# Performance work log

Measured on AMD Instinct MI355X. Metric: run time of the kernel, lower is better.

## Reference

```python
import jax, jax.numpy as jnp
import numpy as np

B, V, C, A = 32, 48, 24, 6
NC, D, H, OUT = 10000, 128, 128, 167


def setup_inputs() -> dict:
    key = jax.random.key(0)
    ks = jax.random.split(key, 12)
    seqs = jax.random.randint(ks[0], (B, V, C), 0, NC + 1)
    ancestors = jax.random.randint(ks[1], (B, V, C, A), 0, NC + 1)
    length = jax.random.randint(ks[2], (B,), 1, V + 1)
    amask = (jax.random.uniform(ks[3], (B, V, C, A)) < 0.7).astype(jnp.float32)
    amask = amask.at[..., 0].set(1.0)  # first ancestor always valid
    emb = jax.random.normal(ks[4], (NC + 1, D), dtype=jnp.float32) * 0.02
    emb = emb.at[NC].set(0.0)  # padding row is zeros
    w_basic = jax.random.normal(ks[5], (D, 2 * D), dtype=jnp.float32) * (1.0 / np.sqrt(2 * D))
    u_basic_w = jax.random.normal(ks[6], (1, D), dtype=jnp.float32) * (1.0 / np.sqrt(D))
    u_basic_b = jnp.zeros((1,), jnp.float32)
    gru_wih = jax.random.normal(ks[7], (3 * H, D), dtype=jnp.float32) * (1.0 / np.sqrt(H))
    gru_whh = jax.random.normal(ks[8], (3 * H, H), dtype=jnp.float32) * (1.0 / np.sqrt(H))
    gru_bih = jnp.zeros((3 * H,), jnp.float32)
    gru_bhh = jnp.zeros((3 * H,), jnp.float32)
    out_w = jax.random.normal(ks[9], (OUT, H), dtype=jnp.float32) * (1.0 / np.sqrt(H))
    out_b = jnp.zeros((OUT,), jnp.float32)
    return dict(seqs=seqs, ancestors=ancestors, length=length, ancestor_length=amask,
                emb=emb, w_basic=w_basic, u_basic_w=u_basic_w, u_basic_b=u_basic_b,
                gru_wih=gru_wih, gru_whh=gru_whh, gru_bih=gru_bih, gru_bhh=gru_bhh,
                out_w=out_w, out_b=out_b)


def _gram_forward(seqs, ancestors, length, ancestor_length, emb, w_basic,
                  u_basic_w, u_basic_b, gru_wih, gru_whh, gru_bih, gru_bhh,
                  out_w, out_b):
    # gather embeddings
    seqs_e = emb[seqs]            # [B,V,C,D]
    anc_e = emb[ancestors]        # [B,V,C,A,D]
    seqs_rep = jnp.broadcast_to(seqs_e[..., None, :], anc_e.shape)
    # Bahdanau attention: mask applied to concat BEFORE the linear (as in source)
    cat = jnp.concatenate([seqs_rep, anc_e], axis=-1) * ancestor_length[..., None]  # [B,V,C,A,2D]
    hdd = jnp.tanh(jnp.einsum('bvcad,ed->bvcae', cat, w_basic))  # [B,V,C,A,D]
    score = jnp.einsum('bvcad,od->bvcao', hdd, u_basic_w) + u_basic_b  # [B,V,C,A,1]
    # mask_softmax over ancestor axis, faithful to the source (sum==0 -> -1)
    e = jnp.exp(score) * ancestor_length[..., None]
    s = jnp.sum(e, axis=3, keepdims=True)
    s = jnp.where(s == 0, -1.0, s)
    attn = e / s                  # [B,V,C,A,1]
    ctx = jnp.sum(attn * anc_e, axis=3)            # [B,V,C,D] weighted ancestor sum
    x = jnp.tanh(jnp.sum(ctx, axis=2))             # [B,V,D] visit embedding

    # single-layer GRU over visits (valid steps form a prefix, padded tail masked below)
    hsz = gru_whh.shape[1]
    def step(hstate, xt):
        gi = xt @ gru_wih.T + gru_bih              # [B,3H]
        gh = hstate @ gru_whh.T + gru_bhh
        ir, iz, inn = jnp.split(gi, 3, axis=-1)
        hr, hz, hn = jnp.split(gh, 3, axis=-1)
        r = jax.nn.sigmoid(ir + hr)
        z = jax.nn.sigmoid(iz + hz)
        n = jnp.tanh(inn + r * hn)
        hnew = (1.0 - z) * n + z * hstate
        return hnew, hnew
    h0 = jnp.zeros((x.shape[0], hsz), x.dtype)
    _, outs = jax.lax.scan(step, h0, jnp.swapaxes(x, 0, 1))  # [V,B,H]
    outs = jnp.swapaxes(outs, 0, 1)                          # [B,V,H]

    visit_mask = (jnp.arange(x.shape[1])[None, :] < length[:, None]).astype(x.dtype)
    context = jnp.einsum('bv,bvh->bh', visit_mask, outs)     # masked sum over visits
    logit = jax.nn.sigmoid(context @ out_w.T + out_b)        # dropout=eval (identity)
    return logit


def reference(seqs, ancestors, length, ancestor_length, emb, w_basic, u_basic_w,
              u_basic_b, gru_wih, gru_whh, gru_bih, gru_bhh, out_w, out_b):
    return _gram_forward(seqs, ancestors, length, ancestor_length, emb, w_basic,
                         u_basic_w, u_basic_b, gru_wih, gru_whh, gru_bih, gru_bhh,
                         out_w, out_b)
```

## Files before the change

### kernel.cpp

```cpp
#include <hip/hip_runtime.h>

#define BB 32
#define VV 48
#define CC 24
#define AA 6
#define NCODES 10001
#define DD 128
#define HH 128
#define OUTN 167
#define G3 384

typedef float f32x4 __attribute__((ext_vector_type(4)));

__device__ __forceinline__ float fast_tanh(float x) {
    return 1.0f - 2.0f / (1.0f + __expf(2.0f * x));
}
__device__ __forceinline__ float fast_sigmoid(float x) {
    return 1.0f / (1.0f + __expf(-x));
}
__device__ __forceinline__ float dot4(float4 a, float4 b) {
    return a.x * b.x + a.y * b.y + a.z * b.z + a.w * b.w;
}
__device__ __forceinline__ float dot4v(f32x4 a, f32x4 b) {
    return a.x * b.x + a.y * b.y + a.z * b.z + a.w * b.w;
}

__global__ __launch_bounds__(256) void k_precompute(
    const float* __restrict__ emb, const float* __restrict__ w_basic,
    float* __restrict__ P1, float* __restrict__ P2, int nrows)
{
    int row0 = blockIdx.x * 16;
    int t = threadIdx.x;
    int tc = t & 127, grp = t >> 7;
    int rbase = row0 + grp * 8;
    const float4* w4 = (const float4*)w_basic;
    const float4* e4 = (const float4*)emb;
    float a0[8] = {}, a1[8] = {};
#pragma unroll 2
    for (int d4 = 0; d4 < 32; ++d4) {
        float4 wv0 = w4[tc * 64 + d4];
        float4 wv1 = w4[tc * 64 + 32 + d4];
#pragma unroll
        for (int r = 0; r < 8; ++r) {
            int row = rbase + r;
            if (row >= nrows) row = nrows - 1;
            float4 ev = e4[row * 32 + d4];
            a0[r] += dot4(ev, wv0);
            a1[r] += dot4(ev, wv1);
        }
    }
#pragma unroll
    for (int r = 0; r < 8; ++r) {
        int row = rbase + r;
        if (row < nrows) {
            P1[row * 128 + tc] = a0[r];
            P2[row * 128 + tc] = a1[r];
        }
    }
}

__global__ __launch_bounds__(256) void k_attention(
    const int* __restrict__ seqs, const int* __restrict__ ancestors,
    const float* __restrict__ amask, const float* __restrict__ emb,
    const float* __restrict__ P1, const float* __restrict__ P2,
    const float* __restrict__ u_w, const float* __restrict__ u_b,
    float* __restrict__ x_out)
{
    __shared__ __align__(16) float u_s[128];
    __shared__ float sc_s[144];
    __shared__ float m_s[144];
    __shared__ int   anc_s[144];
    __shared__ float attn_s[144];
    __shared__ float sum_s[24];
    __shared__ float xred[256];
    int bv = blockIdx.x;
    int t = threadIdx.x;
    if (t < 128) u_s[t] = u_w[t];
    __syncthreads();
    float ub = u_b[0];
    int g = t >> 2, l = t & 3;
    for (int p = g; p < CC * AA; p += 64) {
        int c = p / AA, a = p - c * AA;
        int sidx = bv * CC + c;
        int s_code = seqs[sidx];
        int aidx = sidx * AA + a;
        int anc = ancestors[aidx];
        float m = amask[aidx];
        const float4* p14 = (const float4*)(P1 + s_code * 128);
        const float4* p24 = (const float4*)(P2 + anc * 128);
        const float4* u4 = (const float4*)u_s;
        float partial = 0.0f;
        int e4 = l * 8;
#pragma unroll 2
        for (int j = 0; j < 8; ++j) {
            float4 av = p14[e4 + j];
            float4 bv_ = p24[e4 + j];
            float4 uv = u4[e4 + j];
            partial += fast_tanh(m * (av.x + bv_.x)) * uv.x;
            partial += fast_tanh(m * (av.y + bv_.y)) * uv.y;
            partial += fast_tanh(m * (av.z + bv_.z)) * uv.z;
            partial += fast_tanh(m * (av.w + bv_.w)) * uv.w;
        }
        partial += __shfl_xor(partial, 1);
        partial += __shfl_xor(partial, 2);
        if (l == 0) {
            sc_s[p] = partial + ub;
            m_s[p] = m;
            anc_s[p] = anc;
        }
    }
    __syncthreads();
    if (t < CC * AA) attn_s[t] = __expf(sc_s[t]) * m_s[t];
    __syncthreads();
    if (t < CC) {
        float s = 0.0f;
#pragma unroll
        for (int a = 0; a < AA; ++a) s += attn_s[t * AA + a];
        sum_s[t] = (s == 0.0f) ? -1.0f : s;
    }
    __syncthreads();
    if (t < CC * AA) attn_s[t] = attn_s[t] / sum_s[t / AA];
    __syncthreads();
    int e = t & 127, hc = t >> 7;
    float acc = 0.0f;
    for (int c = hc * 12; c < hc * 12 + 12; ++c) {
#pragma unroll
        for (int a = 0; a < AA; ++a) {
            int p = c * AA + a;
            acc += attn_s[p] * emb[anc_s[p] * 128 + e];
        }
    }
    xred[t] = acc;
    __syncthreads();
    if (t < 128) {
        x_out[bv * 128 + t] = fast_tanh(xred[t] + xred[t + 128]);
    }
}

__global__ __launch_bounds__(384) void k_gi(
    const float* __restrict__ x, const float* __restrict__ wih,
    const float* __restrict__ bih, float* __restrict__ gi)
{
    int row0 = blockIdx.x * 8;
    int t = threadIdx.x;
    const float4* w4 = (const float4*)(wih + t * 128);
    const float4* x4 = (const float4*)(x + row0 * 128);
    float acc[8] = {};
#pragma unroll 2
    for (int d4 = 0; d4 < 32; ++d4) {
        float4 wv = w4[d4];
#pragma unroll
        for (int r = 0; r < 8; ++r) {
            acc[r] += dot4(x4[r * 32 + d4], wv);
        }
    }
    float bb = bih[t];
#pragma unroll
    for (int r = 0; r < 8; ++r) gi[(row0 + r) * G3 + t] = acc[r] + bb;
}

#define GL4(dst, base, OFF) \
    asm volatile("global_load_dwordx4 %0, %1, off offset:" #OFF \
                 : "=v"(dst) : "v"(base))

__global__ __launch_bounds__(256, 1) void k_gru(
    const float* __restrict__ gi, const float* __restrict__ whh,
    const float* __restrict__ bhh, const int* __restrict__ length,
    const float* __restrict__ out_w, const float* __restrict__ out_b,
    float* __restrict__ out)
{
    __shared__ __align__(16) float gl[24 * G3];
    __shared__ __align__(16) float hs[2][128];
    __shared__ __align__(16) float ctxs[128];
    int b = blockIdx.x;
    int t = threadIdx.x;
    int o = t >> 1, half = t & 1;

    const f32x4* bwr = (const f32x4*)(whh + o * 128 + half * 64);
    const f32x4* bwz = (const f32x4*)(whh + (128 + o) * 128 + half * 64);
    const f32x4* bwn = (const f32x4*)(whh + (256 + o) * 128 + half * 64);

    f32x4 wr0, wr1, wr2, wr3, wr4, wr5, wr6, wr7,
          wr8, wr9, wr10, wr11, wr12, wr13, wr14, wr15;
    f32x4 wz0, wz1, wz2, wz3, wz4, wz5, wz6, wz7,
          wz8, wz9, wz10, wz11, wz12, wz13, wz14, wz15;
    f32x4 wn0, wn1, wn2, wn3, wn4, wn5, wn6, wn7,
          wn8, wn9, wn10, wn11, wn12, wn13, wn14, wn15;

    GL4(wr0,  bwr, 0);   GL4(wr1,  bwr, 16);  GL4(wr2,  bwr, 32);  GL4(wr3,  bwr, 48);
    GL4(wr4,  bwr, 64);  GL4(wr5,  bwr, 80);  GL4(wr6,  bwr, 96);  GL4(wr7,  bwr, 112);
    GL4(wr8,  bwr, 128); GL4(wr9,  bwr, 144); GL4(wr10, bwr, 160); GL4(wr11, bwr, 176);
    GL4(wr12, bwr, 192); GL4(wr13, bwr, 208); GL4(wr14, bwr, 224); GL4(wr15, bwr, 240);
    GL4(wz0,  bwz, 0);   GL4(wz1,  bwz, 16);  GL4(wz2,  bwz, 32);  GL4(wz3,  bwz, 48);
    GL4(wz4,  bwz, 64);  GL4(wz5,  bwz, 80);  GL4(wz6,  bwz, 96);  GL4(wz7,  bwz, 112);
    GL4(wz8,  bwz, 128); GL4(wz9,  bwz, 144); GL4(wz10, bwz, 160); GL4(wz11, bwz, 176);
    GL4(wz12, bwz, 192); GL4(wz13, bwz, 208); GL4(wz14, bwz, 224); GL4(wz15, bwz, 240);
    GL4(wn0,  bwn, 0);   GL4(wn1,  bwn, 16);  GL4(wn2,  bwn, 32);  GL4(wn3,  bwn, 48);
    GL4(wn4,  bwn, 64);  GL4(wn5,  bwn, 80);  GL4(wn6,  bwn, 96);  GL4(wn7,  bwn, 112);
    GL4(wn8,  bwn, 128); GL4(wn9,  bwn, 144); GL4(wn10, bwn, 160); GL4(wn11, bwn, 176);
    GL4(wn12, bwn, 192); GL4(wn13, bwn, 208); GL4(wn14, bwn, 224); GL4(wn15, bwn, 240);

    const float4* gib4 = (const float4*)(gi + b * VV * G3);
    {
        float4* dst = (float4*)gl;
#pragma unroll
        for (int i = 0; i < 9; ++i) dst[t + i * 256] = gib4[t + i * 256];
    }

    float bhr = 0.f, bhz = 0.f, bhn = 0.f;
    if (half == 0) {
        bhr = bhh[o];
        bhz = bhh[128 + o];
        bhn = bhh[256 + o];
    }
    if (t < 128) hs[0][t] = 0.0f;
    int len = length[b];
    float ctx = 0.0f;

    asm volatile("s_waitcnt vmcnt(0)" ::: "memory");
    __builtin_amdgcn_sched_barrier(0);
    __syncthreads();

#define STEP2(J, A, B_) do {                                          \
        f32x4 hA = h4[J]; f32x4 hB = h4[J + 1];                       \
        ar0 += dot4v(wr##A, hA);  ar1 += dot4v(wr##B_, hB);           \
        az0 += dot4v(wz##A, hA);  az1 += dot4v(wz##B_, hB);           \
        an0 += dot4v(wn##A, hA);  an1 += dot4v(wn##B_, hB);           \
    } while (0)

    int cur = 0;
    for (int v = 0; v < VV; ++v) {
        if (v == 24) {
            float4* dst = (float4*)gl;
            const float4* src = gib4 + 2304;
#pragma unroll
            for (int i = 0; i < 9; ++i) dst[t + i * 256] = src[t + i * 256];
            __syncthreads();
        }
        int vv = (v >= 24) ? (v - 24) : v;
        float gir = 0.f, giz = 0.f, gin = 0.f;
        if (half == 0) {
            const float* g = gl + vv * G3;
            gir = g[o]; giz = g[128 + o]; gin = g[256 + o];
        }
        const f32x4* h4 = ((const f32x4*)hs[cur]) + half * 16;
        float ar0 = 0.f, ar1 = 0.f, az0 = 0.f, az1 = 0.f, an0 = 0.f, an1 = 0.f;
        STEP2(0, 0, 1);   STEP2(2, 2, 3);    STEP2(4, 4, 5);    STEP2(6, 6, 7);
        STEP2(8, 8, 9);   STEP2(10, 10, 11); STEP2(12, 12, 13); STEP2(14, 14, 15);
        float ar = ar0 + ar1;
        float az = az0 + az1;
        float an = an0 + an1;
        ar += __shfl_xor(ar, 1);
        az += __shfl_xor(az, 1);
        an += __shfl_xor(an, 1);
        if (half == 0) {
            float r = fast_sigmoid(gir + ar + bhr);
            float z = fast_sigmoid(giz + az + bhz);
            float n = fast_tanh(gin + r * (an + bhn));
            float hold = hs[cur][o];
            float hnew = (1.0f - z) * n + z * hold;
            hs[cur ^ 1][o] = hnew;
            if (v < len) ctx += hnew;
        }
        cur ^= 1;
        __syncthreads();
    }
#undef STEP2

    if (half == 0) ctxs[o] = ctx;
    __syncthreads();
    if (t < OUTN) {
        const float4* w4 = (const float4*)(out_w + t * 128);
        const float4* c4 = (const float4*)ctxs;
        float a0 = 0.f, a1 = 0.f;
#pragma unroll 2
        for (int j = 0; j < 32; j += 2) {
            a0 += dot4(w4[j], c4[j]);
            a1 += dot4(w4[j + 1], c4[j + 1]);
        }
        out[b * OUTN + t] = fast_sigmoid(a0 + a1 + out_b[t]);
    }
}

extern "C" void kernel_launch(void* const* d_in, const int* in_sizes, int n_in,
                              void* d_out, int out_size, void* d_ws, size_t ws_size,
                              hipStream_t stream) {
    const int*   seqs      = (const int*)d_in[0];
    const int*   ancestors = (const int*)d_in[1];
    const int*   length    = (const int*)d_in[2];
    const float* amask     = (const float*)d_in[3];
    const float* emb       = (const float*)d_in[4];
    const float* w_basic   = (const float*)d_in[5];
    const float* u_w       = (const float*)d_in[6];
    const float* u_b       = (const float*)d_in[7];
    const float* wih       = (const float*)d_in[8];
    const float* whh       = (const float*)d_in[9];
    const float* bih       = (const float*)d_in[10];
    const float* bhh       = (const float*)d_in[11];
    const float* out_w     = (const float*)d_in[12];
    const float* out_b     = (const float*)d_in[13];
    float* out = (float*)d_out;

    float* ws = (float*)d_ws;
    float* P1 = ws;
    float* P2 = P1 + NCODES * 128;
    float* x  = P2 + NCODES * 128;
    float* gi = x + BB * VV * 128;

    k_precompute<<<(NCODES + 15) / 16, 256, 0, stream>>>(emb, w_basic, P1, P2, NCODES);
    k_attention<<<BB * VV, 256, 0, stream>>>(seqs, ancestors, amask, emb, P1, P2, u_w, u_b, x);
    k_gi<<<(BB * VV) / 8, 384, 0, stream>>>(x, wih, bih, gi);
    k_gru<<<BB, 256, 0, stream>>>(gi, whh, bhh, length, out_w, out_b, out);
}
```

Measured before the change: 164.3 us.

## Stage embeddings in LDS, skip masked ancestors, split GRU matvec across 512 threads

k_precompute now loads the 16 embedding rows into shared memory once instead of every thread re-reading them from global memory. k_attention skips the score computation, P1/P2 gathers and embedding gather for ancestors whose mask is zero, which should be about 30% of them. k_gru moves to 512 threads with four lanes per output row, halving per-thread weight registers and the serial dot-product length on the recurrent critical path, at the cost of an extra shuffle round and more threads per barrier. The masked-skip path is equivalent because masked entries contribute zero attention weight.

Result: faster. 135.0 us (-17.8%).

```diff
diff --git a/kernel.cpp b/kernel.cpp
--- a/kernel.cpp
+++ b/kernel.cpp
@@ -29,32 +29,38 @@
     const float* __restrict__ emb, const float* __restrict__ w_basic,
     float* __restrict__ P1, float* __restrict__ P2, int nrows)
 {
+    __shared__ float4 embs4[16 * 32];
     int row0 = blockIdx.x * 16;
     int t = threadIdx.x;
-    int tc = t & 127, grp = t >> 7;
-    int rbase = row0 + grp * 8;
-    const float4* w4 = (const float4*)w_basic;
-    const float4* e4 = (const float4*)emb;
+    for (int i = t; i < 512; i += 256) {
+        int r = i >> 5;
+        int row = row0 + r;
+        float4 v = make_float4(0.f, 0.f, 0.f, 0.f);
+        if (row < nrows) v = ((const float4*)emb)[row * 32 + (i & 31)];
+        embs4[i] = v;
+    }
+    __syncthreads();
+    int e = t & 127, grp = t >> 7;
+    const float4* w1 = (const float4*)(w_basic + e * 256);
+    const float4* w2 = (const float4*)(w_basic + e * 256 + 128);
     float a0[8] = {}, a1[8] = {};
 #pragma unroll 2
     for (int d4 = 0; d4 < 32; ++d4) {
-        float4 wv0 = w4[tc * 64 + d4];
-        float4 wv1 = w4[tc * 64 + 32 + d4];
+        float4 wv1 = w1[d4];
+        float4 wv2 = w2[d4];
 #pragma unroll
         for (int r = 0; r < 8; ++r) {
-            int row = rbase + r;
-            if (row >= nrows) row = nrows - 1;
-            float4 ev = e4[row * 32 + d4];
-            a0[r] += dot4(ev, wv0);
-            a1[r] += dot4(ev, wv1);
+            float4 ev = embs4[(grp * 8 + r) * 32 + d4];
+            a0[r] += dot4(ev, wv1);
+            a1[r] += dot4(ev, wv2);
         }
     }
 #pragma unroll
     for (int r = 0; r < 8; ++r) {
-        int row = rbase + r;
+        int row = row0 + grp * 8 + r;
         if (row < nrows) {
-            P1[row * 128 + tc] = a0[r];
-            P2[row * 128 + tc] = a1[r];
+            P1[row * 128 + e] = a0[r];
+            P2[row * 128 + e] = a1[r];
         }
     }
 }
@@ -82,35 +88,39 @@
     for (int p = g; p < CC * AA; p += 64) {
         int c = p / AA, a = p - c * AA;
         int sidx = bv * CC + c;
-        int s_code = seqs[sidx];
         int aidx = sidx * AA + a;
         int anc = ancestors[aidx];
         float m = amask[aidx];
-        const float4* p14 = (const float4*)(P1 + s_code * 128);
-        const float4* p24 = (const float4*)(P2 + anc * 128);
-        const float4* u4 = (const float4*)u_s;
-        float partial = 0.0f;
-        int e4 = l * 8;
+        if (l == 0) { m_s[p] = m; anc_s[p] = anc; }
+        if (m != 0.0f) {
+            int s_code = seqs[sidx];
+            const float4* p14 = (const float4*)(P1 + s_code * 128);
+            const float4* p24 = (const float4*)(P2 + anc * 128);
+            const float4* u4 = (const float4*)u_s;
+            float partial = 0.0f;
+            int e4 = l * 8;
 #pragma unroll 2
-        for (int j = 0; j < 8; ++j) {
-            float4 av = p14[e4 + j];
-            float4 bv_ = p24[e4 + j];
-            float4 uv = u4[e4 + j];
-            partial += fast_tanh(m * (av.x + bv_.x)) * uv.x;
-            partial += fast_tanh(m * (av.y + bv_.y)) * uv.y;
-            partial += fast_tanh(m * (av.z + bv_.z)) * uv.z;
-            partial += fast_tanh(m * (av.w + bv_.w)) * uv.w;
-        }
-        partial += __shfl_xor(partial, 1);
-        partial += __shfl_xor(partial, 2);
-        if (l == 0) {
-            sc_s[p] = partial + ub;
-            m_s[p] = m;
-            anc_s[p] = anc;
-        }
-    }
-    __syncthreads();
-    if (t < CC * AA) attn_s[t] = __expf(sc_s[t]) * m_s[t];
+            for (int j = 0; j < 8; ++j) {
+                float4 av = p14[e4 + j];
+                float4 bv_ = p24[e4 + j];
+                float4 uv = u4[e4 + j];
+                partial += fast_tanh(m * (av.x + bv_.x)) * uv.x;
+                partial += fast_tanh(m * (av.y + bv_.y)) * uv.y;
+                partial += fast_tanh(m * (av.z + bv_.z)) * uv.z;
+                partial += fast_tanh(m * (av.w + bv_.w)) * uv.w;
+            }
+            partial += __shfl_xor(partial, 1);
+            partial += __shfl_xor(partial, 2);
+            if (l == 0) sc_s[p] = partial + ub;
+        } else {
+            if (l == 0) sc_s[p] = 0.0f;
+        }
+    }
+    __syncthreads();
+    if (t < CC * AA) {
+        float m = m_s[t];
+        attn_s[t] = (m != 0.0f) ? __expf(sc_s[t]) * m : 0.0f;
+    }
     __syncthreads();
     if (t < CC) {
         float s = 0.0f;
@@ -127,7 +137,8 @@
 #pragma unroll
         for (int a = 0; a < AA; ++a) {
             int p = c * AA + a;
-            acc += attn_s[p] * emb[anc_s[p] * 128 + e];
+            float at = attn_s[p];
+            if (at != 0.0f) acc += at * emb[anc_s[p] * 128 + e];
         }
     }
     xred[t] = acc;
@@ -163,7 +174,7 @@
     asm volatile("global_load_dwordx4 %0, %1, off offset:" #OFF \
                  : "=v"(dst) : "v"(base))
 
-__global__ __launch_bounds__(256, 1) void k_gru(
+__global__ __launch_bounds__(512, 1) void k_gru(
     const float* __restrict__ gi, const float* __restrict__ whh,
     const float* __restrict__ bhh, const int* __restrict__ length,
     const float* __restrict__ out_w, const float* __restrict__ out_b,
@@ -174,41 +185,35 @@
     __shared__ __align__(16) float ctxs[128];
     int b = blockIdx.x;
     int t = threadIdx.x;
-    int o = t >> 1, half = t & 1;
-
-    const f32x4* bwr = (const f32x4*)(whh + o * 128 + half * 64);
-    const f32x4* bwz = (const f32x4*)(whh + (128 + o) * 128 + half * 64);
-    const f32x4* bwn = (const f32x4*)(whh + (256 + o) * 128 + half * 64);
-
-    f32x4 wr0, wr1, wr2, wr3, wr4, wr5, wr6, wr7,
-          wr8, wr9, wr10, wr11, wr12, wr13, wr14, wr15;
-    f32x4 wz0, wz1, wz2, wz3, wz4, wz5, wz6, wz7,
-          wz8, wz9, wz10, wz11, wz12, wz13, wz14, wz15;
-    f32x4 wn0, wn1, wn2, wn3, wn4, wn5, wn6, wn7,
-          wn8, wn9, wn10, wn11, wn12, wn13, wn14, wn15;
-
-    GL4(wr0,  bwr, 0);   GL4(wr1,  bwr, 16);  GL4(wr2,  bwr, 32);  GL4(wr3,  bwr, 48);
-    GL4(wr4,  bwr, 64);  GL4(wr5,  bwr, 80);  GL4(wr6,  bwr, 96);  GL4(wr7,  bwr, 112);
-    GL4(wr8,  bwr, 128); GL4(wr9,  bwr, 144); GL4(wr10, bwr, 160); GL4(wr11, bwr, 176);
-    GL4(wr12, bwr, 192); GL4(wr13, bwr, 208); GL4(wr14, bwr, 224); GL4(wr15, bwr, 240);
-    GL4(wz0,  bwz, 0);   GL4(wz1,  bwz, 16);  GL4(wz2,  bwz, 32);  GL4(wz3,  bwz, 48);
-    GL4(wz4,  bwz, 64);  GL4(wz5,  bwz, 80);  GL4(wz6,  bwz, 96);  GL4(wz7,  bwz, 112);
-    GL4(wz8,  bwz, 128); GL4(wz9,  bwz, 144); GL4(wz10, bwz, 160); GL4(wz11, bwz, 176);
-    GL4(wz12, bwz, 192); GL4(wz13, bwz, 208); GL4(wz14, bwz, 224); GL4(wz15, bwz, 240);
-    GL4(wn0,  bwn, 0);   GL4(wn1,  bwn, 16);  GL4(wn2,  bwn, 32);  GL4(wn3,  bwn, 48);
-    GL4(wn4,  bwn, 64);  GL4(wn5,  bwn, 80);  GL4(wn6,  bwn, 96);  GL4(wn7,  bwn, 112);
-    GL4(wn8,  bwn, 128); GL4(wn9,  bwn, 144); GL4(wn10, bwn, 160); GL4(wn11, bwn, 176);
-    GL4(wn12, bwn, 192); GL4(wn13, bwn, 208); GL4(wn14, bwn, 224); GL4(wn15, bwn, 240);
+    int o = t >> 2, q = t & 3;
+
+    const f32x4* bwr = (const f32x4*)(whh + o * 128 + q * 32);
+    const f32x4* bwz = (const f32x4*)(whh + (128 + o) * 128 + q * 32);
+    const f32x4* bwn = (const f32x4*)(whh + (256 + o) * 128 + q * 32);
+
+    f32x4 wr0, wr1, wr2, wr3, wr4, wr5, wr6, wr7;
+    f32x4 wz0, wz1, wz2, wz3, wz4, wz5, wz6, wz7;
+    f32x4 wn0, wn1, wn2, wn3, wn4, wn5, wn6, wn7;
+
+    GL4(wr0, bwr, 0);  GL4(wr1, bwr, 16); GL4(wr2, bwr, 32); GL4(wr3, bwr, 48);
+    GL4(wr4, bwr, 64); GL4(wr5, bwr, 80); GL4(wr6, bwr, 96); GL4(wr7, bwr, 112);
+    GL4(wz0, bwz, 0);  GL4(wz1, bwz, 16); GL4(wz2, bwz, 32); GL4(wz3, bwz, 48);
+    GL4(wz4, bwz, 64); GL4(wz5, bwz, 80); GL4(wz6, bwz, 96); GL4(wz7, bwz, 112);
+    GL4(wn0, bwn, 0);  GL4(wn1, bwn, 16); GL4(wn2, bwn, 32); GL4(wn3, bwn, 48);
+    GL4(wn4, bwn, 64); GL4(wn5, bwn, 80); GL4(wn6, bwn, 96); GL4(wn7, bwn, 112);
 
     const float4* gib4 = (const float4*)(gi + b * VV * G3);
     {
         float4* dst = (float4*)gl;
 #pragma unroll
-        for (int i = 0; i < 9; ++i) dst[t + i * 256] = gib4[t + i * 256];
+        for (int i = 0; i < 5; ++i) {
+            int idx = t + i * 512;
+            if (idx < 2304) dst[idx] = gib4[idx];
+        }
     }
 
     float bhr = 0.f, bhz = 0.f, bhn = 0.f;
-    if (half == 0) {
+    if (q == 0) {
         bhr = bhh[o];
         bhz = bhh[128 + o];
         bhn = bhh[256 + o];
@@ -221,11 +226,11 @@
     __builtin_amdgcn_sched_barrier(0);
     __syncthreads();
 
-#define STEP2(J, A, B_) do {                                          \
-        f32x4 hA = h4[J]; f32x4 hB = h4[J + 1];                       \
-        ar0 += dot4v(wr##A, hA);  ar1 += dot4v(wr##B_, hB);           \
-        az0 += dot4v(wz##A, hA);  az1 += dot4v(wz##B_, hB);           \
-        an0 += dot4v(wn##A, hA);  an1 += dot4v(wn##B_, hB);           \
+#define STEPJ(J) do {                                                  \
+        f32x4 hv = h4[J];                                              \
+        ar += dot4v(wr##J, hv);                                        \
+        az += dot4v(wz##J, hv);                                        \
+        an += dot4v(wn##J, hv);                                        \
     } while (0)
 
     int cur = 0;
@@ -234,26 +239,29 @@
             float4* dst = (float4*)gl;
             const float4* src = gib4 + 2304;
 #pragma unroll
-            for (int i = 0; i < 9; ++i) dst[t + i * 256] = src[t + i * 256];
+            for (int i = 0; i < 5; ++i) {
+                int idx = t + i * 512;
+                if (idx < 2304) dst[idx] = src[idx];
+            }
             __syncthreads();
         }
         int vv = (v >= 24) ? (v - 24) : v;
         float gir = 0.f, giz = 0.f, gin = 0.f;
-        if (half == 0) {
+        if (q == 0) {
             const float* g = gl + vv * G3;
             gir = g[o]; giz = g[128 + o]; gin = g[256 + o];
         }
-        const f32x4* h4 = ((const f32x4*)hs[cur]) + half * 16;
-        float ar0 = 0.f, ar1 = 0.f, az0 = 0.f, az1 = 0.f, an0 = 0.f, an1 = 0.f;
-        STEP2(0, 0, 1);   STEP2(2, 2, 3);    STEP2(4, 4, 5);    STEP2(6, 6, 7);
-        STEP2(8, 8, 9);   STEP2(10, 10, 11); STEP2(12, 12, 13); STEP2(14, 14, 15);
-        float ar = ar0 + ar1;
-        float az = az0 + az1;
-        float an = an0 + an1;
+        const f32x4* h4 = ((const f32x4*)hs[cur]) + q * 8;
+        float ar = 0.f, az = 0.f, an = 0.f;
+        STEPJ(0); STEPJ(1); STEPJ(2); STEPJ(3);
+        STEPJ(4); STEPJ(5); STEPJ(6); STEPJ(7);
         ar += __shfl_xor(ar, 1);
         az += __shfl_xor(az, 1);
         an += __shfl_xor(an, 1);
-        if (half == 0) {
+        ar += __shfl_xor(ar, 2);
+        az += __shfl_xor(az, 2);
+        an += __shfl_xor(an, 2);
+        if (q == 0) {
             float r = fast_sigmoid(gir + ar + bhr);
             float z = fast_sigmoid(giz + az + bhz);
             float n = fast_tanh(gin + r * (an + bhn));
@@ -265,9 +273,9 @@
         cur ^= 1;
         __syncthreads();
     }
-#undef STEP2
-
-    if (half == 0) ctxs[o] = ctx;
+#undef STEPJ
+
+    if (q == 0) ctxs[o] = ctx;
     __syncthreads();
     if (t < OUTN) {
         const float4* w4 = (const float4*)(out_w + t * 128);
@@ -310,5 +318,5 @@
     k_precompute<<<(NCODES + 15) / 16, 256, 0, stream>>>(emb, w_basic, P1, P2, NCODES);
     k_attention<<<BB * VV, 256, 0, stream>>>(seqs, ancestors, amask, emb, P1, P2, u_w, u_b, x);
     k_gi<<<(BB * VV) / 8, 384, 0, stream>>>(x, wih, bih, gi);
-    k_gru<<<BB, 256, 0, stream>>>(gi, whh, bhh, length, out_w, out_b, out);
-}
+    k_gru<<<BB, 512, 0, stream>>>(gi, whh, bhh, length, out_w, out_b, out);
+}
```
